# Kernel tuning notes

Hardware: AMD Instinct MI355X
Metric: run time of the kernel (lower is better)

## Reference

```python
import jax, jax.numpy as jnp
import numpy as np

MODES = 16   # hard-coded in FNO(..., modes=16, width=32)
WIDTH = 32


def setup_inputs() -> dict:
    key = jax.random.key(0)
    ks = jax.random.split(key, 13)
    B, S, IN, E, OUT, L = 4, 256, 1024, 2048, 1024, 4
    s = 0.02
    return {
        "x": jax.random.normal(ks[0], (B, S, IN), jnp.float32),
        "W_en": jax.random.normal(ks[1], (IN, E), jnp.float32) * s,
        "b_en": jnp.zeros((E,), jnp.float32),
        "fc0_w": jax.random.normal(ks[2], (L, 1, WIDTH), jnp.float32) * s,
        "fc0_b": jnp.zeros((L, WIDTH), jnp.float32),
        "spec_wr": jax.random.normal(ks[3], (L, WIDTH, WIDTH, MODES), jnp.float32) / WIDTH,
        "spec_wi": jax.random.normal(ks[4], (L, WIDTH, WIDTH, MODES), jnp.float32) / WIDTH,
        "pw_w": jax.random.normal(ks[5], (L, WIDTH, WIDTH), jnp.float32) * s,
        "pw_b": jnp.zeros((L, WIDTH), jnp.float32),
        "fc1_w": jax.random.normal(ks[6], (L, WIDTH, 1), jnp.float32) * s,
        "fc1_b": jnp.zeros((L, 1), jnp.float32),
        "W_de": jax.random.normal(ks[7], (E, OUT), jnp.float32) * s,
        "b_de": jnp.zeros((OUT,), jnp.float32),
    }


def _fno_block(u, fc0_w, fc0_b, wr, wi, pw_w, pw_b, fc1_w, fc1_b):
    # u: (T, E, 1) -- 1 channel over spatial axis E
    v = u @ fc0_w + fc0_b                       # (T, E, WIDTH) channel lift
    Vf = jnp.fft.rfft(v, axis=1)                # (T, E//2+1, WIDTH) complex
    Wc = wr + 1j * wi                           # (WIDTH, WIDTH, MODES)
    out_m = jnp.einsum("tmc,cdm->tmd", Vf[:, :MODES, :], Wc)
    Of = jnp.zeros_like(Vf).at[:, :MODES, :].set(out_m)
    v1 = jnp.fft.irfft(Of, n=v.shape[1], axis=1)  # spectral conv branch
    v2 = v @ pw_w + pw_b                          # pointwise 1x1 conv branch
    v = jax.nn.gelu(v1 + v2)
    return v @ fc1_w + fc1_b                      # (T, E, 1) channel project


def reference(x, W_en, b_en, fc0_w, fc0_b, spec_wr, spec_wi, pw_w, pw_b, fc1_w, fc1_b, W_de, b_de):
    h = x @ W_en + b_en                          # (B, S, E)
    B, S, E = h.shape
    u = h.reshape(B * S, E, 1)                   # embed axis = FNO spatial axis, 1 channel
    L = fc0_w.shape[0]
    for i in range(L):                           # small fixed layer count
        u = _fno_block(u, fc0_w[i], fc0_b[i], spec_wr[i], spec_wi[i],
                       pw_w[i], pw_b[i], fc1_w[i], fc1_b[i])
    h = u.reshape(B, S, E)
    return h @ W_de + b_de                       # (B, S, OUT)
```

## Files before the change

kernel.cpp:

```cpp
#include <hip/hip_runtime.h>
#include <math.h>

#ifndef M_PI
#define M_PI 3.14159265358979323846
#endif

#define T_ROWS 1024
#define EDIM   2048
#define IN_DIM 1024
#define OUT_DIM 1024
#define NMODES 16
#define NLAYERS 4

typedef __attribute__((ext_vector_type(8))) short bf16x8;
typedef __attribute__((ext_vector_type(4))) float f32x4;

__device__ __forceinline__ unsigned short f2bf(float f) {
  union { float f; unsigned u; } v; v.f = f;
  unsigned r = v.u + 0x7FFFu + ((v.u >> 16) & 1u);
  return (unsigned short)(r >> 16);
}
__device__ __forceinline__ float bf2f(unsigned short h) {
  union { unsigned u; float f; } v; v.u = ((unsigned)h) << 16;
  return v.f;
}
__device__ __forceinline__ void f2bf_split(float v, unsigned short& h, unsigned short& l) {
  h = f2bf(v);
  l = f2bf(v - bf2f(h));
}

__device__ __forceinline__ void transpose_tile(const float* __restrict__ B,
                                               unsigned short* __restrict__ BT,
                                               int K, int N, int k0, int n0, int tid,
                                               float (*tile)[33])
{
  {
    int r = tid >> 3, c4 = (tid & 7) * 4;
    float4 v = *(const float4*)&B[(size_t)(k0 + r) * N + n0 + c4];
    tile[r][c4 + 0] = v.x; tile[r][c4 + 1] = v.y;
    tile[r][c4 + 2] = v.z; tile[r][c4 + 3] = v.w;
  }
  __syncthreads();
  {
    int n = tid >> 3, kq = (tid & 7) * 4;
    ushort4 o;
    o.x = f2bf(tile[kq + 0][n]); o.y = f2bf(tile[kq + 1][n]);
    o.z = f2bf(tile[kq + 2][n]); o.w = f2bf(tile[kq + 3][n]);
    *(ushort4*)&BT[(size_t)(n0 + n) * K + k0 + kq] = o;
  }
}

__global__ __launch_bounds__(256)
void setup_all(float* __restrict__ ctab, float* __restrict__ stab,
               unsigned short* __restrict__ basFh, unsigned short* __restrict__ basFl,
               const float* __restrict__ fc0w, const float* __restrict__ fc0b,
               const float* __restrict__ wr, const float* __restrict__ wi,
               const float* __restrict__ pww, const float* __restrict__ pwb,
               float* __restrict__ Wmr, float* __restrict__ Wmi,
               float* __restrict__ b0r, float* __restrict__ pw1,
               float* __restrict__ pb1,
               const float* __restrict__ W_en, unsigned short* __restrict__ WenT,
               const float* __restrict__ W_de, unsigned short* __restrict__ WdeT,
               const float* __restrict__ x, unsigned short* __restrict__ x_bf)
{
  __shared__ float tile[32][33];
  const int b = blockIdx.x, tid = threadIdx.x;
  if (b < 8) {
    int i = b * 256 + tid;
    double ang = (2.0 * M_PI / (double)EDIM) * (double)i;
    ctab[i] = (float)cos(ang);
    stab[i] = (float)sin(ang);
  } else if (b < 264) {
    int idx = (b - 8) * 256 + tid;
    int mt = idx >> 9;
    int l  = (idx >> 3) & 63;
    int i  = idx & 7;
    int xx = mt * 16 + (l & 15);
    int j  = (l >> 4) * 8 + i;
    float v;
    if (j < 31) {
      int m = (j < NMODES) ? j : (j - 15);
      int ia = (m * xx) & (EDIM - 1);
      double ang = (2.0 * M_PI / (double)EDIM) * (double)ia;
      v = (j < NMODES) ? (float)cos(ang) : (float)sin(ang);
    } else {
      v = 1.0f;
    }
    unsigned short h, lo; f2bf_split(v, h, lo);
    basFh[idx] = h; basFl[idx] = lo;
  } else if (b == 264) {
    if (tid >= NLAYERS * 32) return;
    int l = tid >> 5, d = tid & 31;
    for (int m = 0; m < NMODES; ++m) {
      float sr = 0.f, si = 0.f;
      for (int c = 0; c < 32; ++c) {
        float w0 = fc0w[l * 32 + c];
        size_t base = ((size_t)(l * 32 + c) * 32 + d) * NMODES + m;
        sr += w0 * wr[base];
        si += w0 * wi[base];
      }
      Wmr[(l * NMODES + m) * 32 + d] = sr;
      Wmi[(l * NMODES + m) * 32 + d] = si;
    }
    float sb = 0.f, sp = 0.f, sq = 0.f;
    for (int c = 0; c < 32; ++c) {
      float b0 = fc0b[l * 32 + c];
      float w0 = fc0w[l * 32 + c];
      sb += b0 * wr[((size_t)(l * 32 + c) * 32 + d) * NMODES + 0];
      float pw = pww[(size_t)(l * 32 + c) * 32 + d];
      sp += w0 * pw;
      sq += b0 * pw;
    }
    b0r[l * 32 + d] = (float)EDIM * sb;
    pw1[l * 32 + d] = sp;
    pb1[l * 32 + d] = sq + pwb[l * 32 + d];
  } else if (b < 2313) {
    int tb = b - 265;
    int n0 = (tb & 63) * 32, k0 = (tb >> 6) * 32;
    transpose_tile(W_en, WenT, IN_DIM, EDIM, k0, n0, tid, tile);
  } else if (b < 4361) {
    int tb = b - 2313;
    int n0 = (tb & 31) * 32, k0 = (tb >> 5) * 32;
    transpose_tile(W_de, WdeT, EDIM, OUT_DIM, k0, n0, tid, tile);
  } else {
    size_t i0 = ((size_t)(b - 4361) * 256 + tid) * 8;
    float4 a0 = *(const float4*)&x[i0];
    float4 a1 = *(const float4*)&x[i0 + 4];
    ushort4 o0, o1;
    o0.x = f2bf(a0.x); o0.y = f2bf(a0.y); o0.z = f2bf(a0.z); o0.w = f2bf(a0.w);
    o1.x = f2bf(a1.x); o1.y = f2bf(a1.y); o1.z = f2bf(a1.z); o1.w = f2bf(a1.w);
    *(ushort4*)&x_bf[i0]     = o0;
    *(ushort4*)&x_bf[i0 + 4] = o1;
  }
}

#define BKK 64
__global__ __launch_bounds__(256)
void gemm_mfma(const unsigned short* __restrict__ A, const unsigned short* __restrict__ BT,
               const float* __restrict__ bias, float* __restrict__ C,
               int M, int N, int K)
{
  __shared__ __align__(16) unsigned short Asb[64 * BKK];
  __shared__ __align__(16) unsigned short Bsb[64 * BKK];
  const int tid = threadIdx.x;
  const int bm = blockIdx.y * 64, bn = blockIdx.x * 64;
  const int lane = tid & 63, wave = tid >> 6;
  const int wr = wave >> 1, wc = wave & 1;

  const int srow = tid >> 2;
  const int skq  = tid & 3;

  f32x4 acc[2][2] = {};

  const unsigned short* aRow = A + (size_t)(bm + srow) * K + skq * 16;
  const unsigned short* bRow = BT + (size_t)(bn + srow) * K + skq * 16;

  for (int k0 = 0; k0 < K; k0 += BKK) {
    #pragma unroll
    for (int h = 0; h < 2; ++h) {
      int kb = skq * 2 + h;
      int slot = kb ^ ((srow >> 1) & 7);
      *(bf16x8*)&Asb[srow * BKK + slot * 8] = *(const bf16x8*)(aRow + k0 + h * 8);
      *(bf16x8*)&Bsb[srow * BKK + slot * 8] = *(const bf16x8*)(bRow + k0 + h * 8);
    }
    __syncthreads();
    #pragma unroll
    for (int s = 0; s < 2; ++s) {
      int kb = s * 4 + (lane >> 4);
      bf16x8 a[2], b[2];
      #pragma unroll
      for (int i = 0; i < 2; ++i) {
        int ar = wr * 32 + i * 16 + (lane & 15);
        a[i] = *(const bf16x8*)&Asb[ar * BKK + (kb ^ ((ar >> 1) & 7)) * 8];
        int br = wc * 32 + i * 16 + (lane & 15);
        b[i] = *(const bf16x8*)&Bsb[br * BKK + (kb ^ ((br >> 1) & 7)) * 8];
      }
      #pragma unroll
      for (int i = 0; i < 2; ++i)
        #pragma unroll
        for (int j = 0; j < 2; ++j)
          acc[i][j] = __builtin_amdgcn_mfma_f32_16x16x32_bf16(a[i], b[j], acc[i][j], 0, 0, 0);
    }
    __syncthreads();
  }

  #pragma unroll
  for (int j = 0; j < 2; ++j) {
    int col = bn + wc * 32 + j * 16 + (lane & 15);
    float bz = bias[col];
    #pragma unroll
    for (int i = 0; i < 2; ++i)
      #pragma unroll
      for (int r = 0; r < 4; ++r) {
        int row = bm + wr * 32 + i * 16 + (lane >> 4) * 4 + r;
        C[(size_t)row * N + col] = acc[i][j][r] + bz;
      }
  }
}

__global__ __launch_bounds__(256)
void dft_coef(const float* __restrict__ u,
              const float* __restrict__ ctab, const float* __restrict__ stab,
              const float* __restrict__ Wmr, const float* __restrict__ Wmi,
              const float* __restrict__ b0r, const float* __restrict__ pb1,
              unsigned short* __restrict__ coefFh, unsigned short* __restrict__ coefFl)
{
  const int t = blockIdx.x, tid = threadIdx.x;
  __shared__ float dred[32][264];
  __shared__ float Ush[32];

  float pr[NMODES], pi[NMODES];
  #pragma unroll
  for (int m = 0; m < NMODES; ++m) { pr[m] = 0.f; pi[m] = 0.f; }
  #pragma unroll
  for (int it = 0; it < 8; ++it) {
    const int x = tid + it * 256;
    const float val = u[(size_t)t * EDIM + x];
    const float cx = ctab[x], sx = stab[x];
    float c = 1.f, s = 0.f;
    #pragma unroll
    for (int m = 0; m < NMODES; ++m) {
      pr[m] += val * c;
      pi[m] -= val * s;
      float cn = c * cx - s * sx;
      s = s * cx + c * sx;
      c = cn;
    }
  }
  #pragma unroll
  for (int m = 0; m < NMODES; ++m) {
    dred[m][tid]          = pr[m];
    dred[NMODES + m][tid] = pi[m];
  }
  __syncthreads();
  {
    const int ch = tid >> 3, p = tid & 7;
    float4 s4 = make_float4(0.f, 0.f, 0.f, 0.f);
    #pragma unroll
    for (int j = 0; j < 8; ++j) {
      const float4 v = *(const float4*)&dred[ch][j * 32 + p * 4];
      s4.x += v.x; s4.y += v.y; s4.z += v.z; s4.w += v.w;
    }
    float ssum = (s4.x + s4.y) + (s4.z + s4.w);
    ssum += __shfl_down(ssum, 4, 64);
    ssum += __shfl_down(ssum, 2, 64);
    ssum += __shfl_down(ssum, 1, 64);
    if (p == 0) Ush[ch] = ssum;
  }
  __syncthreads();

  if (tid < 128) {
    const float invN = 1.0f / (float)EDIM;
    int n = tid >> 6, l = tid & 63;
    int d = n * 16 + (l & 15);
    union { unsigned short u[8]; bf16x8 v; } ph, pl;
    #pragma unroll
    for (int i = 0; i < 8; ++i) {
      int j = (l >> 4) * 8 + i;
      float v;
      if (j < NMODES) {
        int m = j;
        float ofr = Ush[m] * Wmr[m * 32 + d] - Ush[NMODES + m] * Wmi[m * 32 + d];
        v = (m == 0) ? (ofr + b0r[d]) * invN : 2.0f * ofr * invN;
      } else if (j < 31) {
        int m = j - 15;
        float ofi = Ush[m] * Wmi[m * 32 + d] + Ush[NMODES + m] * Wmr[m * 32 + d];
        v = -2.0f * ofi * invN;
      } else {
        v = pb1[d];
      }
      f2bf_split(v, ph.u[i], pl.u[i]);
    }
    size_t base = ((size_t)t * 2 + n) * 64 + l;
    *(bf16x8*)&coefFh[base * 8] = ph.v;
    *(bf16x8*)&coefFl[base * 8] = pl.v;
  }
}

template<int LAST>
__global__ __launch_bounds__(256, 8)
void recon_mfma(float* __restrict__ u,
                unsigned short* __restrict__ u_bf,
                const unsigned short* __restrict__ basFh,
                const unsigned short* __restrict__ basFl,
                const unsigned short* __restrict__ coefFh,
                const unsigned short* __restrict__ coefFl,
                const float* __restrict__ pw1,
                const float* __restrict__ f1w, const float* __restrict__ f1b)
{
  const int t  = blockIdx.x >> 2;
  const int cq = blockIdx.x & 3;
  const int tid = threadIdx.x, lane = tid & 63, w = tid >> 6;
  const int g = lane >> 4, m15 = lane & 15;

  bf16x8 ch[2], cl[2];
  #pragma unroll
  for (int n = 0; n < 2; ++n) {
    size_t base = (((size_t)t * 2 + n) * 64 + lane) * 8;
    ch[n] = *(const bf16x8*)&coefFh[base];
    cl[n] = *(const bf16x8*)&coefFl[base];
  }

  float4 pwv[2], fv[2];
  #pragma unroll
  for (int n = 0; n < 2; ++n) {
    pwv[n] = *(const float4*)&pw1[n * 16 + g * 4];
    fv[n]  = *(const float4*)&f1w[n * 16 + g * 4];
  }
  const float fb = f1b[0];
  float* __restrict__ urow = u + (size_t)t * EDIM;

  #pragma unroll 2
  for (int c2 = 0; c2 < 2; ++c2) {
    #pragma unroll
    for (int q = 0; q < 4; ++q) {
      const int mt = cq * 32 + w * 8 + c2 * 4 + q;
      bf16x8 bh = *(const bf16x8*)&basFh[((size_t)mt * 64 + lane) * 8];
      bf16x8 bl = *(const bf16x8*)&basFl[((size_t)mt * 64 + lane) * 8];
      f32x4 acc[2];
      #pragma unroll
      for (int n = 0; n < 2; ++n) {
        f32x4 a = {};
        a = __builtin_amdgcn_mfma_f32_16x16x32_bf16(cl[n], bh, a, 0, 0, 0);
        a = __builtin_amdgcn_mfma_f32_16x16x32_bf16(ch[n], bl, a, 0, 0, 0);
        a = __builtin_amdgcn_mfma_f32_16x16x32_bf16(ch[n], bh, a, 0, 0, 0);
        acc[n] = a;
      }
      const int x = mt * 16 + m15;
      const float uval = urow[x];
      float o = 0.f;
      #pragma unroll
      for (int n = 0; n < 2; ++n) {
        #pragma unroll
        for (int r = 0; r < 4; ++r) {
          float s = fmaf(uval, ((const float*)&pwv[n])[r], acc[n][r]);
          float s2 = s * s;
          float arg = s * fmaf(0.1029433f, s2, 2.3022082f);
          float e2 = __builtin_amdgcn_exp2f(arg);
          float r1 = __builtin_amdgcn_rcpf(e2 + 1.0f);
          float sf = s * ((const float*)&fv[n])[r];
          o += sf;
          o = fmaf(-sf, r1, o);
        }
      }
      o += __shfl_xor(o, 16, 64);
      o += __shfl_xor(o, 32, 64);
      if (lane < 16) {
        if (LAST) u_bf[(size_t)t * EDIM + x] = f2bf(o + fb);
        else      urow[x] = o + fb;
      }
    }
  }
}

extern "C" void kernel_launch(void* const* d_in, const int* in_sizes, int n_in,
                              void* d_out, int out_size, void* d_ws, size_t ws_size,
                              hipStream_t stream)
{
  const float* x    = (const float*)d_in[0];
  const float* W_en = (const float*)d_in[1];
  const float* b_en = (const float*)d_in[2];
  const float* fc0w = (const float*)d_in[3];
  const float* fc0b = (const float*)d_in[4];
  const float* swr  = (const float*)d_in[5];
  const float* swi  = (const float*)d_in[6];
  const float* pww  = (const float*)d_in[7];
  const float* pwb  = (const float*)d_in[8];
  const float* f1w  = (const float*)d_in[9];
  const float* f1b  = (const float*)d_in[10];
  const float* W_de = (const float*)d_in[11];
  const float* b_de = (const float*)d_in[12];
  float* out = (float*)d_out;
  float* ws  = (float*)d_ws;

  float* u    = ws;
  float* ctab = u + (size_t)T_ROWS * EDIM;
  float* stab = ctab + EDIM;
  float* Wmr  = stab + EDIM;
  float* Wmi  = Wmr + NLAYERS * NMODES * 32;
  float* b0r  = Wmi + NLAYERS * NMODES * 32;
  float* pw1  = b0r + NLAYERS * 32;
  float* pb1  = pw1 + NLAYERS * 32;
  unsigned short* basFh  = (unsigned short*)(pb1 + NLAYERS * 32);
  unsigned short* basFl  = basFh + 128 * 64 * 8;
  unsigned short* coefFh = basFl + 128 * 64 * 8;
  unsigned short* coefFl = coefFh + (size_t)T_ROWS * 2 * 64 * 8;
  unsigned short* x_bf   = coefFl + (size_t)T_ROWS * 2 * 64 * 8;
  unsigned short* u_bf   = x_bf + (size_t)T_ROWS * IN_DIM;
  unsigned short* WenT   = u_bf + (size_t)T_ROWS * EDIM;
  unsigned short* WdeT   = WenT + (size_t)EDIM * IN_DIM;

  setup_all<<<4873, 256, 0, stream>>>(ctab, stab, basFh, basFl, fc0w, fc0b,
                                      swr, swi, pww, pwb, Wmr, Wmi, b0r, pw1, pb1,
                                      W_en, WenT, W_de, WdeT, x, x_bf);

  { dim3 g(EDIM / 64, T_ROWS / 64);
    gemm_mfma<<<g, 256, 0, stream>>>(x_bf, WenT, b_en, u, T_ROWS, EDIM, IN_DIM); }

  for (int l = 0; l < NLAYERS; ++l) {
    dft_coef<<<T_ROWS, 256, 0, stream>>>(u, ctab, stab,
        Wmr + l * NMODES * 32, Wmi + l * NMODES * 32, b0r + l * 32, pb1 + l * 32,
        coefFh, coefFl);
    if (l < NLAYERS - 1)
      recon_mfma<0><<<4 * T_ROWS, 256, 0, stream>>>(u, u_bf, basFh, basFl,
          coefFh, coefFl, pw1 + l * 32, f1w + l * 32, f1b + l);
    else
      recon_mfma<1><<<4 * T_ROWS, 256, 0, stream>>>(u, u_bf, basFh, basFl,
          coefFh, coefFl, pw1 + l * 32, f1w + l * 32, f1b + l);
  }

  { dim3 g(OUT_DIM / 64, T_ROWS / 64);
    gemm_mfma<<<g, 256, 0, stream>>>(u_bf, WdeT, b_de, out, T_ROWS, OUT_DIM, EDIM); }
}
```

Baseline: 240.7 us.

## Fold DFT using half-period symmetry and process two rows per recon block

The DFT coefficient kernel pairs samples x and x+1024 into sum and difference terms. Even modes use the sum and odd modes the difference, which halves the loads and the inner loop trip count. The reconstruction kernel now handles two rows per block, reusing each loaded basis fragment for both rows, and the grid is halved to match. The cost is more registers per thread in recon, which may lower occupancy.

New measurement: 246.4 us. 2.3% more time.

```diff
diff --git a/kernel.cpp b/kernel.cpp
--- a/kernel.cpp
+++ b/kernel.cpp
@@ -213,15 +213,18 @@
   #pragma unroll
   for (int m = 0; m < NMODES; ++m) { pr[m] = 0.f; pi[m] = 0.f; }
   #pragma unroll
-  for (int it = 0; it < 8; ++it) {
+  for (int it = 0; it < 4; ++it) {
     const int x = tid + it * 256;
-    const float val = u[(size_t)t * EDIM + x];
+    const float v0 = u[(size_t)t * EDIM + x];
+    const float v1 = u[(size_t)t * EDIM + x + 1024];
+    const float ve = v0 + v1, vo = v0 - v1;
     const float cx = ctab[x], sx = stab[x];
     float c = 1.f, s = 0.f;
     #pragma unroll
     for (int m = 0; m < NMODES; ++m) {
-      pr[m] += val * c;
-      pi[m] -= val * s;
+      const float vsel = (m & 1) ? vo : ve;
+      pr[m] += vsel * c;
+      pi[m] -= vsel * s;
       float cn = c * cx - s * sx;
       s = s * cx + c * sx;
       c = cn;
@@ -288,18 +291,21 @@
                 const float* __restrict__ pw1,
                 const float* __restrict__ f1w, const float* __restrict__ f1b)
 {
-  const int t  = blockIdx.x >> 2;
+  const int tp = blockIdx.x >> 2;
   const int cq = blockIdx.x & 3;
+  const int t0 = tp * 2;
   const int tid = threadIdx.x, lane = tid & 63, w = tid >> 6;
   const int g = lane >> 4, m15 = lane & 15;
 
-  bf16x8 ch[2], cl[2];
-  #pragma unroll
-  for (int n = 0; n < 2; ++n) {
-    size_t base = (((size_t)t * 2 + n) * 64 + lane) * 8;
-    ch[n] = *(const bf16x8*)&coefFh[base];
-    cl[n] = *(const bf16x8*)&coefFl[base];
-  }
+  bf16x8 ch[2][2], cl[2][2];
+  #pragma unroll
+  for (int tt = 0; tt < 2; ++tt)
+    #pragma unroll
+    for (int n = 0; n < 2; ++n) {
+      size_t base = (((size_t)(t0 + tt) * 2 + n) * 64 + lane) * 8;
+      ch[tt][n] = *(const bf16x8*)&coefFh[base];
+      cl[tt][n] = *(const bf16x8*)&coefFl[base];
+    }
 
   float4 pwv[2], fv[2];
   #pragma unroll
@@ -308,7 +314,7 @@
     fv[n]  = *(const float4*)&f1w[n * 16 + g * 4];
   }
   const float fb = f1b[0];
-  float* __restrict__ urow = u + (size_t)t * EDIM;
+  float* __restrict__ urow0 = u + (size_t)t0 * EDIM;
 
   #pragma unroll 2
   for (int c2 = 0; c2 < 2; ++c2) {
@@ -317,37 +323,41 @@
       const int mt = cq * 32 + w * 8 + c2 * 4 + q;
       bf16x8 bh = *(const bf16x8*)&basFh[((size_t)mt * 64 + lane) * 8];
       bf16x8 bl = *(const bf16x8*)&basFl[((size_t)mt * 64 + lane) * 8];
-      f32x4 acc[2];
+      const int x = mt * 16 + m15;
       #pragma unroll
-      for (int n = 0; n < 2; ++n) {
-        f32x4 a = {};
-        a = __builtin_amdgcn_mfma_f32_16x16x32_bf16(cl[n], bh, a, 0, 0, 0);
-        a = __builtin_amdgcn_mfma_f32_16x16x32_bf16(ch[n], bl, a, 0, 0, 0);
-        a = __builtin_amdgcn_mfma_f32_16x16x32_bf16(ch[n], bh, a, 0, 0, 0);
-        acc[n] = a;
-      }
-      const int x = mt * 16 + m15;
-      const float uval = urow[x];
-      float o = 0.f;
-      #pragma unroll
-      for (int n = 0; n < 2; ++n) {
+      for (int tt = 0; tt < 2; ++tt) {
+        f32x4 acc[2];
         #pragma unroll
-        for (int r = 0; r < 4; ++r) {
-          float s = fmaf(uval, ((const float*)&pwv[n])[r], acc[n][r]);
-          float s2 = s * s;
-          float arg = s * fmaf(0.1029433f, s2, 2.3022082f);
-          float e2 = __builtin_amdgcn_exp2f(arg);
-          float r1 = __builtin_amdgcn_rcpf(e2 + 1.0f);
-          float sf = s * ((const float*)&fv[n])[r];
-          o += sf;
-          o = fmaf(-sf, r1, o);
+        for (int n = 0; n < 2; ++n) {
+          f32x4 a = {};
+          a = __builtin_amdgcn_mfma_f32_16x16x32_bf16(cl[tt][n], bh, a, 0, 0, 0);
+          a = __builtin_amdgcn_mfma_f32_16x16x32_bf16(ch[tt][n], bl, a, 0, 0, 0);
+          a = __builtin_amdgcn_mfma_f32_16x16x32_bf16(ch[tt][n], bh, a, 0, 0, 0);
+          acc[n] = a;
         }
-      }
-      o += __shfl_xor(o, 16, 64);
-      o += __shfl_xor(o, 32, 64);
-      if (lane < 16) {
-        if (LAST) u_bf[(size_t)t * EDIM + x] = f2bf(o + fb);
-        else      urow[x] = o + fb;
+        float* __restrict__ up = urow0 + (size_t)tt * EDIM + x;
+        const float uval = *up;
+        float o = 0.f;
+        #pragma unroll
+        for (int n = 0; n < 2; ++n) {
+          #pragma unroll
+          for (int r = 0; r < 4; ++r) {
+            float s = fmaf(uval, ((const float*)&pwv[n])[r], acc[n][r]);
+            float s2 = s * s;
+            float arg = s * fmaf(0.1029433f, s2, 2.3022082f);
+            float e2 = __builtin_amdgcn_exp2f(arg);
+            float r1 = __builtin_amdgcn_rcpf(e2 + 1.0f);
+            float sf = s * ((const float*)&fv[n])[r];
+            o += sf;
+            o = fmaf(-sf, r1, o);
+          }
+        }
+        o += __shfl_xor(o, 16, 64);
+        o += __shfl_xor(o, 32, 64);
+        if (lane < 16) {
+          if (LAST) u_bf[(size_t)(t0 + tt) * EDIM + x] = f2bf(o + fb);
+          else      *up = o + fb;
+        }
       }
     }
   }
@@ -402,10 +412,10 @@
         Wmr + l * NMODES * 32, Wmi + l * NMODES * 32, b0r + l * 32, pb1 + l * 32,
         coefFh, coefFl);
     if (l < NLAYERS - 1)
-      recon_mfma<0><<<4 * T_ROWS, 256, 0, stream>>>(u, u_bf, basFh, basFl,
+      recon_mfma<0><<<2 * T_ROWS, 256, 0, stream>>>(u, u_bf, basFh, basFl,
           coefFh, coefFl, pw1 + l * 32, f1w + l * 32, f1b + l);
     else
-      recon_mfma<1><<<4 * T_ROWS, 256, 0, stream>>>(u, u_bf, basFh, basFl,
+      recon_mfma<1><<<2 * T_ROWS, 256, 0, stream>>>(u, u_bf, basFh, basFl,
           coefFh, coefFl, pw1 + l * 32, f1w + l * 32, f1b + l);
   }
 
```
